# Kernel tuning notes

Hardware: AMD Instinct MI355X
Metric: run time of the kernel (lower is better)

Reference implementation:

```python
import jax, jax.numpy as jnp
import numpy as np

EPS = 1e-5

def _bn_eval(x, gamma, beta, rmean, rvar):
    # BatchNorm1d in eval mode: elementwise affine using running stats
    inv = jax.lax.rsqrt(rvar + EPS)
    return (x - rmean) * inv * gamma + beta

def setup_inputs() -> dict:
    key = jax.random.key(0)
    ks = jax.random.split(key, 12)
    N, F, H, C = 16384, 512, 512, 128
    x = jax.random.normal(ks[0], (N, F), dtype=jnp.float32)
    a = jax.random.uniform(ks[1], (N, N), dtype=jnp.float32)
    w1 = jax.random.normal(ks[2], (F, H), dtype=jnp.float32) * (1.0 / np.sqrt(F))
    b1 = jax.random.normal(ks[3], (H,), dtype=jnp.float32) * 0.01
    w2 = jax.random.normal(ks[4], (H, C), dtype=jnp.float32) * (1.0 / np.sqrt(H))
    b2 = jax.random.normal(ks[5], (C,), dtype=jnp.float32) * 0.01
    g1 = jax.random.normal(ks[6], (F,), dtype=jnp.float32) * 0.1 + 1.0
    beta1 = jax.random.normal(ks[7], (F,), dtype=jnp.float32) * 0.01
    rm1 = jax.random.normal(ks[8], (F,), dtype=jnp.float32) * 0.1
    rv1 = jax.random.uniform(ks[9], (F,), dtype=jnp.float32, minval=0.5, maxval=1.5)
    g2 = jax.random.normal(ks[10], (H,), dtype=jnp.float32) * 0.1 + 1.0
    beta2 = jax.random.normal(ks[11], (H,), dtype=jnp.float32) * 0.01
    rm2 = jnp.zeros((H,), dtype=jnp.float32)
    rv2 = jnp.ones((H,), dtype=jnp.float32)
    return {"x": x, "a": a, "w1": w1, "b1": b1, "w2": w2, "b2": b2,
            "g1": g1, "beta1": beta1, "rm1": rm1, "rv1": rv1,
            "g2": g2, "beta2": beta2, "rm2": rm2, "rv2": rv2}

def reference(x, a, w1, b1, w2, b2, g1, beta1, rm1, rv1, g2, beta2, rm2, rv2):
    # x: [N, F] node features, a: [N, N] adjacency
    x2 = _bn_eval(x, g1, beta1, rm1, rv1)          # norm1
    x2 = a @ x2                                     # message passing (aggregation)
    x2 = x2 @ w1 + b1                               # conv1 (Linear)
    x2 = jax.nn.relu(x2)
    x2 = _bn_eval(x2, g2, beta2, rm2, rv2)          # norm2
    # dropout is identity in eval mode
    x1 = a @ x2                                     # second aggregation
    x1 = x1 @ w2 + b2                               # conv2 (Linear)
    return (x1, x2)
```

## Files before the change

### kernel.cpp

```cpp
#include <hip/hip_runtime.h>
#include <hip/hip_bf16.h>

typedef unsigned short u16;
typedef unsigned int u32;
typedef __attribute__((ext_vector_type(4))) float f32x4;
typedef __attribute__((ext_vector_type(8))) short bf16x8;

#define DEVI static __device__ __forceinline__

DEVI u16 f2bf(float f) {
  u32 u = __builtin_bit_cast(u32, f);
  u += 0x7fffu + ((u >> 16) & 1u);
  return (u16)(u >> 16);
}

DEVI void gload_lds16(const void* g, void* l) {
  __builtin_amdgcn_global_load_lds(
      (const __attribute__((address_space(1))) u32*)g,
      (__attribute__((address_space(3))) u32*)l, 16, 0, 0);
}

template<int BN, int WM, int WN, bool AF32, int EPI>
__global__ __launch_bounds__(512)
void gemm_bt(const void* __restrict__ Ap, const u16* __restrict__ Bt,
             const int K, const int M,
             float* __restrict__ outf, u16* __restrict__ outh,
             const float* __restrict__ e0, const float* __restrict__ e1,
             const float* __restrict__ e2, const float* __restrict__ e3,
             const float* __restrict__ e4)
{
  constexpr int BM = 64, BK = 64;
  static_assert(WM * WN == 8, "8 waves");
  constexpr int TM = BM / WM, TN = BN / WN;
  constexpr int MF = TM / 16, NF = TN / 16;
  constexpr int ABYTES = BM * BK * 2;
  constexpr int BBYTES = BN * BK * 2;

  __shared__ char smem[2 * ABYTES + 2 * BBYTES];

  const int tid = threadIdx.x;
  const int w = tid >> 6, l = tid & 63;
  const int wm = w / WN, wn = w % WN;
  const int l15 = l & 15, l4 = l >> 4;

  const int nwg = gridDim.x;
  const int cpx = nwg >> 3;
  const int bid = blockIdx.x;
  const int wg = (bid & 7) * cpx + (bid >> 3);
  const int m0 = wg * BM;

  const int NT = K / BK;

  const int ar = tid >> 3, ac = tid & 7;
  const int apos = (ar * 128 + ac * 16) ^ ((ar & 7) << 4);
  const size_t Abase = (size_t)(m0 + ar) * K + (size_t)ac * 8;

  f32x4 av0, av1;
  uint4 ah;

  f32x4 acc[MF][NF];
#pragma unroll
  for (int i = 0; i < MF; ++i)
#pragma unroll
    for (int j = 0; j < NF; ++j) acc[i][j] = (f32x4){0.f, 0.f, 0.f, 0.f};

  auto issueA = [&](int t) {
    if constexpr (AF32) {
      const float* p = (const float*)Ap + Abase + (size_t)t * BK;
      av0 = *(const f32x4*)p;
      av1 = *(const f32x4*)(p + 4);
    } else {
      const u16* p = (const u16*)Ap + Abase + (size_t)t * BK;
      ah = *(const uint4*)p;
    }
  };
  auto writeA = [&](int nb) {
    uint4 pk;
    if constexpr (AF32) {
      pk.x = (u32)f2bf(av0[0]) | ((u32)f2bf(av0[1]) << 16);
      pk.y = (u32)f2bf(av0[2]) | ((u32)f2bf(av0[3]) << 16);
      pk.z = (u32)f2bf(av1[0]) | ((u32)f2bf(av1[1]) << 16);
      pk.w = (u32)f2bf(av1[2]) | ((u32)f2bf(av1[3]) << 16);
    } else {
      pk = ah;
    }
    *(uint4*)(smem + nb * ABYTES + apos) = pk;
  };
  auto issueB = [&](int nb, int t) {
    const char* bsrc = (const char*)Bt + (size_t)t * (BK * 2);
    char* bdst = smem + 2 * ABYTES + nb * BBYTES + w * (BBYTES / 8);
#pragma unroll
    for (int j = 0; j < BN / 64; ++j) {
      const int p = w * (BBYTES / 8) + j * 1024 + l * 16;
      const int q = p ^ (((p >> 7) & 7) << 4);
      gload_lds16(bsrc + (size_t)(q >> 7) * ((size_t)K * 2) + (q & 127),
                  bdst + j * 1024);
    }
  };
  auto compute = [&](int cb) {
    const char* A = smem + cb * ABYTES;
    const char* B = smem + 2 * ABYTES + cb * BBYTES;
    bf16x8 af[MF][2], bfv[NF][2];
#pragma unroll
    for (int k2 = 0; k2 < 2; ++k2) {
#pragma unroll
      for (int mi = 0; mi < MF; ++mi) {
        const int row = wm * TM + mi * 16 + l15;
        const int off = (row * 128 + k2 * 64 + l4 * 16) ^ ((row & 7) << 4);
        af[mi][k2] = *(const bf16x8*)(A + off);
      }
#pragma unroll
      for (int ni = 0; ni < NF; ++ni) {
        const int n = wn * TN + ni * 16 + l15;
        const int off = (n * 128 + k2 * 64 + l4 * 16) ^ ((n & 7) << 4);
        bfv[ni][k2] = *(const bf16x8*)(B + off);
      }
    }
#pragma unroll
    for (int k2 = 0; k2 < 2; ++k2)
#pragma unroll
      for (int mi = 0; mi < MF; ++mi)
#pragma unroll
        for (int ni = 0; ni < NF; ++ni)
          acc[mi][ni] = __builtin_amdgcn_mfma_f32_16x16x32_bf16(
              af[mi][k2], bfv[ni][k2], acc[mi][ni], 0, 0, 0);
  };

  issueB(0, 0);
  issueA(0);
  writeA(0);
  __syncthreads();

  for (int t = 0; t < NT; ++t) {
    const int cur = t & 1, nxt = cur ^ 1;
    const bool more = (t + 1 < NT);
    if (more) { issueB(nxt, t + 1); issueA(t + 1); }
    compute(cur);
    if (more) writeA(nxt);
    __syncthreads();
  }

  const int mrow0 = m0 + wm * TM + l4 * 4;
#pragma unroll
  for (int ni = 0; ni < NF; ++ni) {
    const int n = wn * TN + ni * 16 + l15;
    if constexpr (EPI == 0) {
#pragma unroll
      for (int mi = 0; mi < MF; ++mi) {
        const int m = mrow0 + mi * 16;
        ushort4 o;
        o.x = f2bf(acc[mi][ni][0]);
        o.y = f2bf(acc[mi][ni][1]);
        o.z = f2bf(acc[mi][ni][2]);
        o.w = f2bf(acc[mi][ni][3]);
        *(ushort4*)(outh + (size_t)n * M + m) = o;
      }
    } else if constexpr (EPI == 1) {
      const float b1v = e0[n];
      const float sc = e1[n] * rsqrtf(e4[n] + 1e-5f);
      const float sh = e2[n] - e3[n] * sc;
#pragma unroll
      for (int mi = 0; mi < MF; ++mi)
#pragma unroll
        for (int r = 0; r < 4; ++r) {
          const int m = mrow0 + mi * 16 + r;
          float s = acc[mi][ni][r] + b1v;
          s = fmaxf(s, 0.f);
          outf[(size_t)m * BN + n] = s * sc + sh;
        }
    } else {
      const float b2v = e0[n];
#pragma unroll
      for (int mi = 0; mi < MF; ++mi)
#pragma unroll
        for (int r = 0; r < 4; ++r) {
          const int m = mrow0 + mi * 16 + r;
          outf[(size_t)m * BN + n] = acc[mi][ni][r] + b2v;
        }
    }
  }
}

__global__ __launch_bounds__(256)
void bn1_cast_k(const float* __restrict__ x, const float* __restrict__ g,
                const float* __restrict__ be, const float* __restrict__ rm,
                const float* __restrict__ rv, u16* __restrict__ out)
{
  const size_t i8 = ((size_t)blockIdx.x * 256 + threadIdx.x) * 8;
  const f32x4 v0 = *(const f32x4*)(x + i8);
  const f32x4 v1 = *(const f32x4*)(x + i8 + 4);
  const int f0 = (int)(i8 & 511);
  u16 u[8];
#pragma unroll
  for (int e = 0; e < 8; ++e) {
    const int f = f0 + e;
    const float sc = g[f] * rsqrtf(rv[f] + 1e-5f);
    const float v = (e < 4) ? v0[e] : v1[e - 4];
    u[e] = f2bf((v - rm[f]) * sc + be[f]);
  }
  uint4 o;
  o.x = (u32)u[0] | ((u32)u[1] << 16);
  o.y = (u32)u[2] | ((u32)u[3] << 16);
  o.z = (u32)u[4] | ((u32)u[5] << 16);
  o.w = (u32)u[6] | ((u32)u[7] << 16);
  *(uint4*)(out + i8) = o;
}

__global__ __launch_bounds__(256)
void tcvt_k(const float* __restrict__ in, u16* __restrict__ out, int rowlen)
{
  const int o = blockIdx.x * 256 + threadIdx.x;
  const int n = o >> 9, k = o & 511;
  out[o] = f2bf(in[(size_t)k * rowlen + n]);
}

extern "C" void kernel_launch(void* const* d_in, const int* in_sizes, int n_in,
                              void* d_out, int out_size, void* d_ws, size_t ws_size,
                              hipStream_t stream)
{
  const float* x   = (const float*)d_in[0];
  const float* a   = (const float*)d_in[1];
  const float* w1  = (const float*)d_in[2];
  const float* b1  = (const float*)d_in[3];
  const float* w2  = (const float*)d_in[4];
  const float* b2  = (const float*)d_in[5];
  const float* g1  = (const float*)d_in[6];
  const float* be1 = (const float*)d_in[7];
  const float* rm1 = (const float*)d_in[8];
  const float* rv1 = (const float*)d_in[9];
  const float* g2  = (const float*)d_in[10];
  const float* be2 = (const float*)d_in[11];
  const float* rm2 = (const float*)d_in[12];
  const float* rv2 = (const float*)d_in[13];

  constexpr int N = 16384, F = 512, H = 512, C = 128;
  float* out_x1 = (float*)d_out;
  float* out_x2 = (float*)d_out + (size_t)N * C;

  char* wsp = (char*)d_ws;
  u16* xb  = (u16*)wsp;  wsp += (size_t)N * F * 2;
  u16* t_t = (u16*)wsp;  wsp += (size_t)H * N * 2;
  u16* z_t = (u16*)wsp;  wsp += (size_t)C * N * 2;
  u16* w1t = (u16*)wsp;  wsp += (size_t)H * F * 2;
  u16* w2t = (u16*)wsp;  wsp += (size_t)C * H * 2;

  bn1_cast_k<<<(N * F / 8) / 256, 256, 0, stream>>>(x, g1, be1, rm1, rv1, xb);
  tcvt_k<<<(F * H) / 256, 256, 0, stream>>>(w1, w1t, H);
  tcvt_k<<<(H * C) / 256, 256, 0, stream>>>(w2, w2t, C);

  gemm_bt<512, 1, 8, false, 0><<<N / 64, 512, 0, stream>>>(
      xb, w1t, F, N, nullptr, t_t, nullptr, nullptr, nullptr, nullptr, nullptr);

  gemm_bt<512, 1, 8, true, 1><<<N / 64, 512, 0, stream>>>(
      a, t_t, N, N, out_x2, nullptr, b1, g2, be2, rm2, rv2);

  gemm_bt<128, 2, 4, true, 0><<<N / 64, 512, 0, stream>>>(
      out_x2, w2t, H, N, nullptr, z_t, nullptr, nullptr, nullptr, nullptr, nullptr);

  gemm_bt<128, 2, 4, true, 2><<<N / 64, 512, 0, stream>>>(
      a, z_t, N, N, out_x1, nullptr, b2, nullptr, nullptr, nullptr, nullptr);
}
```

Measured before the change: 857.2 us.

## Load B fragments directly to registers and deepen A prefetch pipeline

Replaces the LDS staging of the B operand with per-wave direct global loads into registers, double-buffered across iterations. The wave layout becomes 1x8 along N, so each wave reads only its own B columns, and A is now prefetched two tiles ahead using two register sets. LDS usage drops to the A buffers only, and launch bounds request two blocks per CU to raise occupancy. In exchange, B reads hit L2 from every block without LDS sharing, and register pressure rises.

```diff
diff --git a/kernel.cpp b/kernel.cpp
--- a/kernel.cpp
+++ b/kernel.cpp
@@ -14,14 +14,8 @@
   return (u16)(u >> 16);
 }
 
-DEVI void gload_lds16(const void* g, void* l) {
-  __builtin_amdgcn_global_load_lds(
-      (const __attribute__((address_space(1))) u32*)g,
-      (__attribute__((address_space(3))) u32*)l, 16, 0, 0);
-}
-
-template<int BN, int WM, int WN, bool AF32, int EPI>
-__global__ __launch_bounds__(512)
+template<int BN, bool AF32, int EPI>
+__global__ __launch_bounds__(512, 2)
 void gemm_bt(const void* __restrict__ Ap, const u16* __restrict__ Bt,
              const int K, const int M,
              float* __restrict__ outf, u16* __restrict__ outh,
@@ -30,21 +24,19 @@
              const float* __restrict__ e4)
 {
   constexpr int BM = 64, BK = 64;
-  static_assert(WM * WN == 8, "8 waves");
-  constexpr int TM = BM / WM, TN = BN / WN;
-  constexpr int MF = TM / 16, NF = TN / 16;
+  constexpr int TN = BN / 8;
+  constexpr int MF = BM / 16;
+  constexpr int NF = TN / 16;
   constexpr int ABYTES = BM * BK * 2;
-  constexpr int BBYTES = BN * BK * 2;
-
-  __shared__ char smem[2 * ABYTES + 2 * BBYTES];
+
+  __shared__ char smem[2 * ABYTES];
 
   const int tid = threadIdx.x;
   const int w = tid >> 6, l = tid & 63;
-  const int wm = w / WN, wn = w % WN;
+  const int wn = w;
   const int l15 = l & 15, l4 = l >> 4;
 
-  const int nwg = gridDim.x;
-  const int cpx = nwg >> 3;
+  const int cpx = gridDim.x >> 3;
   const int bid = blockIdx.x;
   const int wg = (bid & 7) * cpx + (bid >> 3);
   const int m0 = wg * BM;
@@ -55,92 +47,98 @@
   const int apos = (ar * 128 + ac * 16) ^ ((ar & 7) << 4);
   const size_t Abase = (size_t)(m0 + ar) * K + (size_t)ac * 8;
 
-  f32x4 av0, av1;
-  uint4 ah;
-
   f32x4 acc[MF][NF];
 #pragma unroll
   for (int i = 0; i < MF; ++i)
 #pragma unroll
     for (int j = 0; j < NF; ++j) acc[i][j] = (f32x4){0.f, 0.f, 0.f, 0.f};
 
-  auto issueA = [&](int t) {
+  struct Aregs { f32x4 v0, v1; uint4 h; };
+  Aregs R0, R1;
+  uint4 BR0[NF][2], BR1[NF][2];
+
+  auto issueA = [&](Aregs& R, int t) {
     if constexpr (AF32) {
       const float* p = (const float*)Ap + Abase + (size_t)t * BK;
-      av0 = *(const f32x4*)p;
-      av1 = *(const f32x4*)(p + 4);
+      R.v0 = *(const f32x4*)p;
+      R.v1 = *(const f32x4*)(p + 4);
     } else {
       const u16* p = (const u16*)Ap + Abase + (size_t)t * BK;
-      ah = *(const uint4*)p;
-    }
-  };
-  auto writeA = [&](int nb) {
+      R.h = *(const uint4*)p;
+    }
+  };
+  auto writeA = [&](int nb, Aregs& R) {
     uint4 pk;
     if constexpr (AF32) {
-      pk.x = (u32)f2bf(av0[0]) | ((u32)f2bf(av0[1]) << 16);
-      pk.y = (u32)f2bf(av0[2]) | ((u32)f2bf(av0[3]) << 16);
-      pk.z = (u32)f2bf(av1[0]) | ((u32)f2bf(av1[1]) << 16);
-      pk.w = (u32)f2bf(av1[2]) | ((u32)f2bf(av1[3]) << 16);
+      pk.x = (u32)f2bf(R.v0[0]) | ((u32)f2bf(R.v0[1]) << 16);
+      pk.y = (u32)f2bf(R.v0[2]) | ((u32)f2bf(R.v0[3]) << 16);
+      pk.z = (u32)f2bf(R.v1[0]) | ((u32)f2bf(R.v1[1]) << 16);
+      pk.w = (u32)f2bf(R.v1[2]) | ((u32)f2bf(R.v1[3]) << 16);
     } else {
-      pk = ah;
+      pk = R.h;
     }
     *(uint4*)(smem + nb * ABYTES + apos) = pk;
   };
-  auto issueB = [&](int nb, int t) {
-    const char* bsrc = (const char*)Bt + (size_t)t * (BK * 2);
-    char* bdst = smem + 2 * ABYTES + nb * BBYTES + w * (BBYTES / 8);
-#pragma unroll
-    for (int j = 0; j < BN / 64; ++j) {
-      const int p = w * (BBYTES / 8) + j * 1024 + l * 16;
-      const int q = p ^ (((p >> 7) & 7) << 4);
-      gload_lds16(bsrc + (size_t)(q >> 7) * ((size_t)K * 2) + (q & 127),
-                  bdst + j * 1024);
-    }
-  };
-  auto compute = [&](int cb) {
+  auto issueB = [&](uint4 (&BR)[NF][2], int t) {
+#pragma unroll
+    for (int ni = 0; ni < NF; ++ni)
+#pragma unroll
+      for (int kk = 0; kk < 2; ++kk) {
+        const int n = wn * TN + ni * 16 + l15;
+        BR[ni][kk] = *(const uint4*)(Bt + (size_t)n * K + (size_t)t * BK +
+                                     kk * 32 + l4 * 8);
+      }
+  };
+  auto compute = [&](int cb, uint4 (&BR)[NF][2]) {
     const char* A = smem + cb * ABYTES;
-    const char* B = smem + 2 * ABYTES + cb * BBYTES;
-    bf16x8 af[MF][2], bfv[NF][2];
-#pragma unroll
-    for (int k2 = 0; k2 < 2; ++k2) {
+#pragma unroll
+    for (int kk = 0; kk < 2; ++kk) {
+      bf16x8 af[MF];
 #pragma unroll
       for (int mi = 0; mi < MF; ++mi) {
-        const int row = wm * TM + mi * 16 + l15;
-        const int off = (row * 128 + k2 * 64 + l4 * 16) ^ ((row & 7) << 4);
-        af[mi][k2] = *(const bf16x8*)(A + off);
+        const int row = mi * 16 + l15;
+        const int off = (row * 128 + kk * 64 + l4 * 16) ^ ((row & 7) << 4);
+        af[mi] = *(const bf16x8*)(A + off);
       }
-#pragma unroll
-      for (int ni = 0; ni < NF; ++ni) {
-        const int n = wn * TN + ni * 16 + l15;
-        const int off = (n * 128 + k2 * 64 + l4 * 16) ^ ((n & 7) << 4);
-        bfv[ni][k2] = *(const bf16x8*)(B + off);
-      }
-    }
-#pragma unroll
-    for (int k2 = 0; k2 < 2; ++k2)
 #pragma unroll
       for (int mi = 0; mi < MF; ++mi)
 #pragma unroll
         for (int ni = 0; ni < NF; ++ni)
           acc[mi][ni] = __builtin_amdgcn_mfma_f32_16x16x32_bf16(
-              af[mi][k2], bfv[ni][k2], acc[mi][ni], 0, 0, 0);
-  };
-
-  issueB(0, 0);
-  issueA(0);
-  writeA(0);
-  __syncthreads();
-
-  for (int t = 0; t < NT; ++t) {
-    const int cur = t & 1, nxt = cur ^ 1;
-    const bool more = (t + 1 < NT);
-    if (more) { issueB(nxt, t + 1); issueA(t + 1); }
-    compute(cur);
-    if (more) writeA(nxt);
-    __syncthreads();
-  }
-
-  const int mrow0 = m0 + wm * TM + l4 * 4;
+              af[mi], __builtin_bit_cast(bf16x8, BR[ni][kk]), acc[mi][ni],
+              0, 0, 0);
+    }
+  };
+
+#define BARRIER() asm volatile("s_waitcnt lgkmcnt(0)\ns_barrier" ::: "memory")
+
+  issueA(R0, 0);
+  issueA(R1, 1);
+  issueB(BR0, 0);
+  writeA(0, R0);
+  BARRIER();
+
+#define STEP(CUR, R_W, R_I, BR_C, BR_I, T)                                   \
+  {                                                                          \
+    const bool haveB = (T) + 1 < NT;                                         \
+    const bool haveA = (T) + 2 < NT;                                         \
+    if (haveB) issueB(BR_I, (T) + 1);                                        \
+    if (haveA) issueA(R_I, (T) + 2);                                         \
+    compute((CUR), BR_C);                                                    \
+    if (haveB) {                                                             \
+      writeA((CUR) ^ 1, R_W);                                                \
+      BARRIER();                                                             \
+    }                                                                        \
+  }
+
+  for (int t = 0; t < NT; t += 2) {
+    STEP(0, R1, R0, BR0, BR1, t);
+    STEP(1, R0, R1, BR1, BR0, t + 1);
+  }
+#undef STEP
+#undef BARRIER
+
+  const int mrow0 = m0 + l4 * 4;
 #pragma unroll
   for (int ni = 0; ni < NF; ++ni) {
     const int n = wn * TN + ni * 16 + l15;
@@ -248,15 +246,15 @@
   tcvt_k<<<(F * H) / 256, 256, 0, stream>>>(w1, w1t, H);
   tcvt_k<<<(H * C) / 256, 256, 0, stream>>>(w2, w2t, C);
 
-  gemm_bt<512, 1, 8, false, 0><<<N / 64, 512, 0, stream>>>(
+  gemm_bt<512, false, 0><<<N / 64, 512, 0, stream>>>(
       xb, w1t, F, N, nullptr, t_t, nullptr, nullptr, nullptr, nullptr, nullptr);
 
-  gemm_bt<512, 1, 8, true, 1><<<N / 64, 512, 0, stream>>>(
+  gemm_bt<512, true, 1><<<N / 64, 512, 0, stream>>>(
       a, t_t, N, N, out_x2, nullptr, b1, g2, be2, rm2, rv2);
 
-  gemm_bt<128, 2, 4, true, 0><<<N / 64, 512, 0, stream>>>(
+  gemm_bt<128, true, 0><<<N / 64, 512, 0, stream>>>(
       out_x2, w2t, H, N, nullptr, z_t, nullptr, nullptr, nullptr, nullptr, nullptr);
 
-  gemm_bt<128, 2, 4, true, 2><<<N / 64, 512, 0, stream>>>(
+  gemm_bt<128, true, 2><<<N / 64, 512, 0, stream>>>(
       a, z_t, N, N, out_x1, nullptr, b2, nullptr, nullptr, nullptr, nullptr);
 }
```

Measured after the change: 935.6 us. 9.2% more time.
